# Performance work log

Measured on AMD Instinct MI355X. Metric: run time of the kernel, lower is better.

## Reference

```python
import jax, jax.numpy as jnp
import numpy as np

D_MODEL, D_K, D_V, H = 512, 64, 64, 8
B, NQ, NK = 2, 2048, 2048


def setup_inputs() -> dict:
    key = jax.random.key(0)
    ks = jax.random.split(key, 12)
    inp = {
        "queries": jax.random.normal(ks[0], (B, NQ, D_MODEL), jnp.float32),
        "keys": jax.random.normal(ks[1], (B, NK, D_MODEL), jnp.float32),
        "values": jax.random.normal(ks[2], (B, NK, D_MODEL), jnp.float32),
        "attention_weights": jax.random.uniform(ks[3], (B, H, NQ, NK), jnp.float32),
        # causal mask: True above the diagonal => masked (every row keeps >=1 entry)
        "attention_mask": jnp.broadcast_to(
            jnp.triu(jnp.ones((NQ, NK), dtype=bool), k=1), (B, H, NQ, NK)
        ),
        # linear params, torch Linear convention: W [out, in], b [out]
        "Wq": 0.001 * jax.random.normal(ks[4], (H * D_K, D_MODEL), jnp.float32),
        "bq": jnp.zeros((H * D_K,), jnp.float32),
        "Wk": 0.001 * jax.random.normal(ks[5], (H * D_K, D_MODEL), jnp.float32),
        "bk": jnp.zeros((H * D_K,), jnp.float32),
        "Wv": 0.001 * jax.random.normal(ks[6], (H * D_V, D_MODEL), jnp.float32),
        "bv": jnp.zeros((H * D_V,), jnp.float32),
        "Wo": 0.001 * jax.random.normal(ks[7], (D_MODEL, H * D_V), jnp.float32),
        "bo": jnp.zeros((D_MODEL,), jnp.float32),
    }
    return inp


def reference(queries, keys, values, attention_weights, attention_mask,
              Wq, bq, Wk, bk, Wv, bv, Wo, bo):
    b_s, nq, _ = queries.shape
    nk = keys.shape[1]
    # projections -> (b, h, n, d)
    q = (queries @ Wq.T + bq).reshape(b_s, nq, H, D_K).transpose(0, 2, 1, 3)
    k = (keys @ Wk.T + bk).reshape(b_s, nk, H, D_K).transpose(0, 2, 1, 3)
    v = (values @ Wv.T + bv).reshape(b_s, nk, H, D_V).transpose(0, 2, 1, 3)
    att = jnp.einsum('bhqd,bhkd->bhqk', q, k) / np.sqrt(D_K).astype(np.float32)
    att = att * attention_weights
    att = jnp.where(attention_mask, -jnp.inf, att)
    att = jax.nn.softmax(att, axis=-1)  # dropout p=0 => identity (eval)
    out = jnp.einsum('bhqk,bhkd->bhqd', att, v)
    out = out.transpose(0, 2, 1, 3).reshape(b_s, nq, H * D_V)
    return out @ Wo.T + bo
```

## Files before the change

kernel.cpp:

```cpp
#include <hip/hip_runtime.h>


typedef unsigned short u16;
typedef unsigned int u32;
typedef __bf16 bf16x8 __attribute__((ext_vector_type(8)));
typedef float f32x4 __attribute__((ext_vector_type(4)));

#define NQTILES 32

__device__ inline u16 f2bf(float f) {
    u32 x = __builtin_bit_cast(u32, f);
    u32 r = (x + 0x7fffu + ((x >> 16) & 1u)) >> 16;
    return (u16)r;
}

__device__ inline f32x4 mfma16(bf16x8 a, bf16x8 b, f32x4 c) {
    return __builtin_amdgcn_mfma_f32_16x16x32_bf16(a, b, c, 0, 0, 0);
}

__device__ inline void gload16(const void* g, void* l) {
    __builtin_amdgcn_global_load_lds((const __attribute__((address_space(1))) void*)g,
                                     (__attribute__((address_space(3))) void*)l, 16, 0, 0);
}

__device__ inline void stage_swz(const u16* __restrict__ src, int ld, int nrows,
                                 char* lds, int tid) {
    int lane = tid & 63;
    int total = nrows * 8;
    for (int p = tid; p < total; p += 256) {
        int row = p >> 3;
        int seg = (p & 7) ^ (row & 7);
        const char* g = (const char*)(src + (size_t)row * ld) + (seg << 4);
        char* l = lds + ((size_t)(p - lane) << 4);
        gload16(g, l);
    }
}

__device__ inline bf16x8 ldsf(const char* lds, int row, int seg) {
    return *(const bf16x8*)(lds + row * 128 + (((seg ^ (row & 7)) & 7) << 4));
}

__device__ inline void loadw(float (&w)[16], const float* __restrict__ wgt, size_t wbase,
                             int q0, int k0, int wrow, int lg, int lc) {
#pragma unroll
    for (int c = 0; c < 4; ++c)
#pragma unroll
        for (int r = 0; r < 4; ++r)
            w[c * 4 + r] =
                wgt[wbase + (size_t)(q0 + wrow + lg * 4 + r) * 2048 + k0 + c * 16 + lc];
}

__global__ __launch_bounds__(256) void convert_kernel(
    const float* __restrict__ q, const float* __restrict__ k, const float* __restrict__ v,
    const float* __restrict__ wq, const float* __restrict__ wk, const float* __restrict__ wv,
    const float* __restrict__ wo, u16* __restrict__ dst) {
    size_t i = ((size_t)blockIdx.x * 256 + threadIdx.x) * 8;
    if (i >= 7340032) return;
    const float* src; size_t off;
    if      (i < 2097152) { src = q;  off = i; }
    else if (i < 4194304) { src = k;  off = i - 2097152; }
    else if (i < 6291456) { src = v;  off = i - 4194304; }
    else if (i < 6553600) { src = wq; off = i - 6291456; }
    else if (i < 6815744) { src = wk; off = i - 6553600; }
    else if (i < 7077888) { src = wv; off = i - 6815744; }
    else                  { src = wo; off = i - 7077888; }
    float4 a = *(const float4*)(src + off);
    float4 b = *(const float4*)(src + off + 4);
    uint4 pk;
    pk.x = f2bf(a.x) | ((u32)f2bf(a.y) << 16);
    pk.y = f2bf(a.z) | ((u32)f2bf(a.w) << 16);
    pk.z = f2bf(b.x) | ((u32)f2bf(b.y) << 16);
    pk.w = f2bf(b.z) | ((u32)f2bf(b.w) << 16);
    *(uint4*)(dst + i) = pk;
}

__device__ inline void gemm_core(const u16* __restrict__ A, const u16* __restrict__ W,
                                 const float* __restrict__ bias,
                                 u16* __restrict__ outB, float* __restrict__ outF,
                                 char (*Alds)[16384], char (*Blds)[16384],
                                 int bx, int by, int tid) {
    const int lane = tid & 63, wid = tid >> 6;
    const int wr = wid >> 1, wc = wid & 1;
    const int lg = lane >> 4, lc = lane & 15;
    const int brow = by * 128, bcol = bx * 128;
    f32x4 acc[4][4] = {};
    stage_swz(A + (size_t)brow * 512, 512, 128, Alds[0], tid);
    stage_swz(W + (size_t)bcol * 512, 512, 128, Blds[0], tid);
    __syncthreads();
    for (int kt = 0; kt < 8; ++kt) {
        const int cur = kt & 1;
        if (kt < 7) {
            stage_swz(A + (size_t)brow * 512 + (kt + 1) * 64, 512, 128, Alds[cur ^ 1], tid);
            stage_swz(W + (size_t)bcol * 512 + (kt + 1) * 64, 512, 128, Blds[cur ^ 1], tid);
        }
#pragma unroll
        for (int s = 0; s < 2; ++s) {
            bf16x8 af[4], bf[4];
#pragma unroll
            for (int m = 0; m < 4; ++m) af[m] = ldsf(Alds[cur], wr * 64 + m * 16 + lc, s * 4 + lg);
#pragma unroll
            for (int n = 0; n < 4; ++n) bf[n] = ldsf(Blds[cur], wc * 64 + n * 16 + lc, s * 4 + lg);
#pragma unroll
            for (int m = 0; m < 4; ++m)
#pragma unroll
                for (int n = 0; n < 4; ++n)
                    acc[m][n] = mfma16(af[m], bf[n], acc[m][n]);
        }
        __syncthreads();
    }
#pragma unroll
    for (int n = 0; n < 4; ++n) {
        int gcol = bcol + wc * 64 + n * 16 + lc;
        float bv = bias[gcol];
#pragma unroll
        for (int m = 0; m < 4; ++m) {
            int grow0 = brow + wr * 64 + m * 16 + lg * 4;
#pragma unroll
            for (int r = 0; r < 4; ++r) {
                float v = acc[m][n][r] + bv;
                if (outF) outF[(size_t)(grow0 + r) * 512 + gcol] = v;
                else      outB[(size_t)(grow0 + r) * 512 + gcol] = f2bf(v);
            }
        }
    }
}

__global__ __launch_bounds__(256, 2) void gemm_qkv_kernel(
    const u16* __restrict__ qx, const u16* __restrict__ kx, const u16* __restrict__ vx,
    const u16* __restrict__ wq, const u16* __restrict__ wk, const u16* __restrict__ wv,
    const float* __restrict__ bq, const float* __restrict__ bk, const float* __restrict__ bv,
    u16* __restrict__ qp, u16* __restrict__ kp, u16* __restrict__ vp) {
    __shared__ __attribute__((aligned(16))) char Alds[2][16384];
    __shared__ __attribute__((aligned(16))) char Blds[2][16384];
    int z = blockIdx.z;
    const u16* A = (z == 0) ? qx : (z == 1) ? kx : vx;
    const u16* W = (z == 0) ? wq : (z == 1) ? wk : wv;
    const float* bias = (z == 0) ? bq : (z == 1) ? bk : bv;
    u16* out = (z == 0) ? qp : (z == 1) ? kp : vp;
    gemm_core(A, W, bias, out, nullptr, Alds, Blds, blockIdx.x, blockIdx.y, threadIdx.x);
}

__global__ __launch_bounds__(256, 2) void gemm_out_kernel(
    const u16* __restrict__ ob, const u16* __restrict__ wo,
    const float* __restrict__ bo, float* __restrict__ out) {
    __shared__ __attribute__((aligned(16))) char Alds[2][16384];
    __shared__ __attribute__((aligned(16))) char Blds[2][16384];
    gemm_core(ob, wo, bo, nullptr, out, Alds, Blds, blockIdx.x, blockIdx.y, threadIdx.x);
}

__global__ __launch_bounds__(256) void vtrans_kernel(const u16* __restrict__ vp,
                                                     u16* __restrict__ vt) {
    __shared__ __attribute__((aligned(16))) u16 t[64 * 64];
    int tid = threadIdx.x, lane = tid & 63;
    int nt = blockIdx.x;
    int bh = blockIdx.y;
    int b = bh >> 3, h = bh & 7;
    for (int ii = 0; ii < 2; ++ii) {
        int p = ii * 256 + tid;
        int nrow = p >> 3, seg = p & 7;
        const char* g = (const char*)(vp + ((size_t)(b * 2048 + nt * 64 + nrow)) * 512 + h * 64)
                        + (seg << 4);
        char* l = (char*)t + ((size_t)(p - lane) << 4);
        gload16(g, l);
    }
    __syncthreads();
    for (int ii = 0; ii < 2; ++ii) {
        int idx = ii * 256 + tid;
        int d = idx >> 3;
        int nseg = idx & 7;
        u16 tmp[8];
#pragma unroll
        for (int j = 0; j < 8; ++j) tmp[j] = t[(nseg * 8 + j) * 64 + d];
        uint4 pk;
        pk.x = tmp[0] | ((u32)tmp[1] << 16);
        pk.y = tmp[2] | ((u32)tmp[3] << 16);
        pk.z = tmp[4] | ((u32)tmp[5] << 16);
        pk.w = tmp[6] | ((u32)tmp[7] << 16);
        *(uint4*)(vt + ((size_t)(bh * 64 + d)) * 2048 + nt * 64 + nseg * 8) = pk;
    }
}

__global__ __launch_bounds__(256, 2) void attn_kernel(
    const u16* __restrict__ qp, const u16* __restrict__ kp, const u16* __restrict__ vt,
    const float* __restrict__ wgt, u16* __restrict__ ob) {
    __shared__ __attribute__((aligned(16))) char kbuf[2][8192];
    __shared__ __attribute__((aligned(16))) char vbuf[2][8192];
    __shared__ __attribute__((aligned(16))) char pbuf[8192];
    const int tid = threadIdx.x, lane = tid & 63, wid = tid >> 6;
    const int lg = lane >> 4, lc = lane & 15;
    const int bid = blockIdx.x;
    const int rank = bid >> 4;
    const int bh = bid & 15;
    const int it = (NQTILES - 1) - rank;
    const int b = bh >> 3, h = bh & 7;
    const int q0 = it * 64;
    const int wrow = wid * 16;
    const size_t wbase = ((size_t)(b * 8 + h)) * 2048 * 2048;
    const size_t vtb0 = ((size_t)(bh * 64)) * 2048;

    stage_swz(qp + ((size_t)(b * 2048 + q0)) * 512 + h * 64, 512, 64, pbuf, tid);
    stage_swz(kp + ((size_t)(b * 2048)) * 512 + h * 64, 512, 64, kbuf[0], tid);
    stage_swz(vt + vtb0, 2048, 64, vbuf[0], tid);
    float wcur[16], wnxt[16];
    loadw(wcur, wgt, wbase, q0, 0, wrow, lg, lc);
#pragma unroll
    for (int i = 0; i < 16; ++i) wnxt[i] = 0.f;
    __syncthreads();
    bf16x8 qf[2];
#pragma unroll
    for (int s = 0; s < 2; ++s) qf[s] = ldsf(pbuf, wrow + lc, s * 4 + lg);

    float mrow[4], lrow[4];
#pragma unroll
    for (int r = 0; r < 4; ++r) { mrow[r] = -1e30f; lrow[r] = 0.f; }
    f32x4 oacc[4] = {};

    for (int j = 0; j <= it; ++j) {
        const int cur = j & 1;
        if (j < it) {
            stage_swz(kp + ((size_t)(b * 2048 + (j + 1) * 64)) * 512 + h * 64, 512, 64,
                      kbuf[cur ^ 1], tid);
            stage_swz(vt + vtb0 + (j + 1) * 64, 2048, 64, vbuf[cur ^ 1], tid);
            loadw(wnxt, wgt, wbase, q0, (j + 1) * 64, wrow, lg, lc);
        }

        f32x4 sacc[4] = {};
#pragma unroll
        for (int s = 0; s < 2; ++s) {
            bf16x8 kf[4];
#pragma unroll
            for (int c = 0; c < 4; ++c) kf[c] = ldsf(kbuf[cur], c * 16 + lc, s * 4 + lg);
#pragma unroll
            for (int c = 0; c < 4; ++c) sacc[c] = mfma16(qf[s], kf[c], sacc[c]);
        }

#pragma unroll
        for (int r = 0; r < 4; ++r) {
            float mx = -1e30f;
#pragma unroll
            for (int c = 0; c < 4; ++c) {
                float sv = sacc[c][r] * 0.125f * wcur[c * 4 + r];
                if (j == it) {
                    int qq = wrow + lg * 4 + r, kk = c * 16 + lc;
                    if (kk > qq) sv = -1e30f;
                }
                sacc[c][r] = sv;
                mx = fmaxf(mx, sv);
            }
            mx = fmaxf(mx, __shfl_xor(mx, 1));
            mx = fmaxf(mx, __shfl_xor(mx, 2));
            mx = fmaxf(mx, __shfl_xor(mx, 4));
            mx = fmaxf(mx, __shfl_xor(mx, 8));
            float mnew = fmaxf(mrow[r], mx);
            float sc = __expf(mrow[r] - mnew);
            float sum = 0.f;
#pragma unroll
            for (int c = 0; c < 4; ++c) {
                float e = __expf(sacc[c][r] - mnew);
                sacc[c][r] = e;
                sum += e;
            }
            sum += __shfl_xor(sum, 1);
            sum += __shfl_xor(sum, 2);
            sum += __shfl_xor(sum, 4);
            sum += __shfl_xor(sum, 8);
            lrow[r] = lrow[r] * sc + sum;
            mrow[r] = mnew;
#pragma unroll
            for (int c = 0; c < 4; ++c) oacc[c][r] *= sc;
        }

#pragma unroll
        for (int c = 0; c < 4; ++c)
#pragma unroll
            for (int r = 0; r < 4; ++r) {
                int row = wrow + lg * 4 + r;
                int byte = (c * 16 + lc) * 2;
                *(u16*)(pbuf + row * 128 + (byte ^ ((row & 7) << 4))) = f2bf(sacc[c][r]);
            }

        bf16x8 pa[2];
#pragma unroll
        for (int s = 0; s < 2; ++s) pa[s] = ldsf(pbuf, wrow + lc, s * 4 + lg);
#pragma unroll
        for (int c = 0; c < 4; ++c)
#pragma unroll
            for (int s = 0; s < 2; ++s) {
                bf16x8 vf = ldsf(vbuf[cur], c * 16 + lc, s * 4 + lg);
                oacc[c] = mfma16(pa[s], vf, oacc[c]);
            }
        __syncthreads();
        if (j < it) {
#pragma unroll
            for (int i = 0; i < 16; ++i) wcur[i] = wnxt[i];
        }
    }

#pragma unroll
    for (int r = 0; r < 4; ++r) {
        float inv = 1.f / lrow[r];
        int qq = q0 + wrow + lg * 4 + r;
        size_t base = ((size_t)(b * 2048 + qq)) * 512 + h * 64;
#pragma unroll
        for (int c = 0; c < 4; ++c)
            ob[base + c * 16 + lc] = f2bf(oacc[c][r] * inv);
    }
}

extern "C" void kernel_launch(void* const* d_in, const int* in_sizes, int n_in,
                              void* d_out, int out_size, void* d_ws, size_t ws_size,
                              hipStream_t stream) {
    const float* q   = (const float*)d_in[0];
    const float* k   = (const float*)d_in[1];
    const float* v   = (const float*)d_in[2];
    const float* wgt = (const float*)d_in[3];
    const float* Wq = (const float*)d_in[5];
    const float* bq = (const float*)d_in[6];
    const float* Wk = (const float*)d_in[7];
    const float* bk = (const float*)d_in[8];
    const float* Wv = (const float*)d_in[9];
    const float* bv = (const float*)d_in[10];
    const float* Wo = (const float*)d_in[11];
    const float* bo = (const float*)d_in[12];
    float* out = (float*)d_out;

    u16* ws  = (u16*)d_ws;
    u16* qx  = ws;
    u16* kx  = qx  + 2097152;
    u16* vx  = kx  + 2097152;
    u16* wqb = vx  + 2097152;
    u16* wkb = wqb + 262144;
    u16* wvb = wkb + 262144;
    u16* wob = wvb + 262144;
    u16* qp  = wob + 262144;
    u16* kp  = qp  + 2097152;
    u16* vp  = kp  + 2097152;
    u16* vtb = vp  + 2097152;
    u16* ob  = vtb + 2097152;

    convert_kernel<<<3584, 256, 0, stream>>>(q, k, v, Wq, Wk, Wv, Wo, qx);
    gemm_qkv_kernel<<<dim3(4, 32, 3), 256, 0, stream>>>(qx, kx, vx, wqb, wkb, wvb,
                                                        bq, bk, bv, qp, kp, vp);
    vtrans_kernel<<<dim3(32, 16), 256, 0, stream>>>(vp, vtb);
    attn_kernel<<<512, 256, 0, stream>>>(qp, kp, vtb, wgt, ob);
    gemm_out_kernel<<<dim3(4, 32, 1), 256, 0, stream>>>(ob, wob, bo, out);
}
```

Baseline: 541.0 us.

## Fuse fp32-to-bf16 conversion and V transpose into projection GEMMs

Removes the separate convert kernel and the V transpose kernel. The QKV and output GEMMs now load fp32 inputs and weights into registers, convert them to bf16, and write the result to swizzled LDS while the MFMAs of the previous tile run. The V projection writes its output directly in transposed layout. This drops two launches and the round trips of the bf16 intermediates through global memory. In exchange it doubles global read bytes inside the GEMMs, raises register pressure, and the transposed V stores are only 8-byte scattered writes.

```diff
diff --git a/kernel.cpp b/kernel.cpp
--- a/kernel.cpp
+++ b/kernel.cpp
@@ -40,6 +40,32 @@
     return *(const bf16x8*)(lds + row * 128 + (((seg ^ (row & 7)) & 7) << 4));
 }
 
+__device__ inline void ldf32(const float* __restrict__ src, int tid, float4 (&h)[8]) {
+#pragma unroll
+    for (int k = 0; k < 4; ++k) {
+        int p = tid + 256 * k;
+        int row = p >> 3, seg = p & 7;
+        const float4* g = (const float4*)(src + (size_t)row * 512 + seg * 8);
+        h[2 * k]     = g[0];
+        h[2 * k + 1] = g[1];
+    }
+}
+
+__device__ inline void wrstage(const float4 (&h)[8], char* lds, int tid) {
+#pragma unroll
+    for (int k = 0; k < 4; ++k) {
+        int p = tid + 256 * k;
+        int row = p >> 3, seg = (p & 7) ^ (row & 7);
+        float4 a = h[2 * k], b = h[2 * k + 1];
+        uint4 pk;
+        pk.x = f2bf(a.x) | ((u32)f2bf(a.y) << 16);
+        pk.y = f2bf(a.z) | ((u32)f2bf(a.w) << 16);
+        pk.z = f2bf(b.x) | ((u32)f2bf(b.y) << 16);
+        pk.w = f2bf(b.z) | ((u32)f2bf(b.w) << 16);
+        *(uint4*)(lds + row * 128 + (seg << 4)) = pk;
+    }
+}
+
 __device__ inline void loadw(float (&w)[16], const float* __restrict__ wgt, size_t wbase,
                              int q0, int k0, int wrow, int lg, int lc) {
 #pragma unroll
@@ -50,48 +76,34 @@
                 wgt[wbase + (size_t)(q0 + wrow + lg * 4 + r) * 2048 + k0 + c * 16 + lc];
 }
 
-__global__ __launch_bounds__(256) void convert_kernel(
+__global__ __launch_bounds__(256, 2) void gemm_qkvt_kernel(
     const float* __restrict__ q, const float* __restrict__ k, const float* __restrict__ v,
     const float* __restrict__ wq, const float* __restrict__ wk, const float* __restrict__ wv,
-    const float* __restrict__ wo, u16* __restrict__ dst) {
-    size_t i = ((size_t)blockIdx.x * 256 + threadIdx.x) * 8;
-    if (i >= 7340032) return;
-    const float* src; size_t off;
-    if      (i < 2097152) { src = q;  off = i; }
-    else if (i < 4194304) { src = k;  off = i - 2097152; }
-    else if (i < 6291456) { src = v;  off = i - 4194304; }
-    else if (i < 6553600) { src = wq; off = i - 6291456; }
-    else if (i < 6815744) { src = wk; off = i - 6553600; }
-    else if (i < 7077888) { src = wv; off = i - 6815744; }
-    else                  { src = wo; off = i - 7077888; }
-    float4 a = *(const float4*)(src + off);
-    float4 b = *(const float4*)(src + off + 4);
-    uint4 pk;
-    pk.x = f2bf(a.x) | ((u32)f2bf(a.y) << 16);
-    pk.y = f2bf(a.z) | ((u32)f2bf(a.w) << 16);
-    pk.z = f2bf(b.x) | ((u32)f2bf(b.y) << 16);
-    pk.w = f2bf(b.z) | ((u32)f2bf(b.w) << 16);
-    *(uint4*)(dst + i) = pk;
-}
-
-__device__ inline void gemm_core(const u16* __restrict__ A, const u16* __restrict__ W,
-                                 const float* __restrict__ bias,
-                                 u16* __restrict__ outB, float* __restrict__ outF,
-                                 char (*Alds)[16384], char (*Blds)[16384],
-                                 int bx, int by, int tid) {
-    const int lane = tid & 63, wid = tid >> 6;
+    const float* __restrict__ bq, const float* __restrict__ bk, const float* __restrict__ bv,
+    u16* __restrict__ qp, u16* __restrict__ kp, u16* __restrict__ vt) {
+    __shared__ __attribute__((aligned(16))) char Alds[2][16384];
+    __shared__ __attribute__((aligned(16))) char Blds[2][16384];
+    const int z = blockIdx.z;
+    const float* A = (z == 0) ? q : (z == 1) ? k : v;
+    const float* W = (z == 0) ? wq : (z == 1) ? wk : wv;
+    const float* bias = (z == 0) ? bq : (z == 1) ? bk : bv;
+    const int tid = threadIdx.x, lane = tid & 63, wid = tid >> 6;
     const int wr = wid >> 1, wc = wid & 1;
     const int lg = lane >> 4, lc = lane & 15;
-    const int brow = by * 128, bcol = bx * 128;
+    const int brow = blockIdx.y * 128, bcol = blockIdx.x * 128;
     f32x4 acc[4][4] = {};
-    stage_swz(A + (size_t)brow * 512, 512, 128, Alds[0], tid);
-    stage_swz(W + (size_t)bcol * 512, 512, 128, Blds[0], tid);
+    float4 ha[8], hw[8];
+
+    ldf32(A + (size_t)brow * 512, tid, ha);
+    ldf32(W + (size_t)bcol * 512, tid, hw);
+    wrstage(ha, Alds[0], tid);
+    wrstage(hw, Blds[0], tid);
     __syncthreads();
     for (int kt = 0; kt < 8; ++kt) {
         const int cur = kt & 1;
         if (kt < 7) {
-            stage_swz(A + (size_t)brow * 512 + (kt + 1) * 64, 512, 128, Alds[cur ^ 1], tid);
-            stage_swz(W + (size_t)bcol * 512 + (kt + 1) * 64, 512, 128, Blds[cur ^ 1], tid);
+            ldf32(A + (size_t)brow * 512 + (kt + 1) * 64, tid, ha);
+            ldf32(W + (size_t)bcol * 512 + (kt + 1) * 64, tid, hw);
         }
 #pragma unroll
         for (int s = 0; s < 2; ++s) {
@@ -106,77 +118,98 @@
                 for (int n = 0; n < 4; ++n)
                     acc[m][n] = mfma16(af[m], bf[n], acc[m][n]);
         }
+        if (kt < 7) {
+            wrstage(ha, Alds[cur ^ 1], tid);
+            wrstage(hw, Blds[cur ^ 1], tid);
+        }
         __syncthreads();
     }
-#pragma unroll
-    for (int n = 0; n < 4; ++n) {
-        int gcol = bcol + wc * 64 + n * 16 + lc;
-        float bv = bias[gcol];
-#pragma unroll
-        for (int m = 0; m < 4; ++m) {
-            int grow0 = brow + wr * 64 + m * 16 + lg * 4;
-#pragma unroll
-            for (int r = 0; r < 4; ++r) {
-                float v = acc[m][n][r] + bv;
-                if (outF) outF[(size_t)(grow0 + r) * 512 + gcol] = v;
-                else      outB[(size_t)(grow0 + r) * 512 + gcol] = f2bf(v);
-            }
-        }
-    }
-}
-
-__global__ __launch_bounds__(256, 2) void gemm_qkv_kernel(
-    const u16* __restrict__ qx, const u16* __restrict__ kx, const u16* __restrict__ vx,
-    const u16* __restrict__ wq, const u16* __restrict__ wk, const u16* __restrict__ wv,
-    const float* __restrict__ bq, const float* __restrict__ bk, const float* __restrict__ bv,
-    u16* __restrict__ qp, u16* __restrict__ kp, u16* __restrict__ vp) {
-    __shared__ __attribute__((aligned(16))) char Alds[2][16384];
-    __shared__ __attribute__((aligned(16))) char Blds[2][16384];
-    int z = blockIdx.z;
-    const u16* A = (z == 0) ? qx : (z == 1) ? kx : vx;
-    const u16* W = (z == 0) ? wq : (z == 1) ? wk : wv;
-    const float* bias = (z == 0) ? bq : (z == 1) ? bk : bv;
-    u16* out = (z == 0) ? qp : (z == 1) ? kp : vp;
-    gemm_core(A, W, bias, out, nullptr, Alds, Blds, blockIdx.x, blockIdx.y, threadIdx.x);
+
+    if (z < 2) {
+        u16* out = (z == 0) ? qp : kp;
+#pragma unroll
+        for (int n = 0; n < 4; ++n) {
+            int gcol = bcol + wc * 64 + n * 16 + lc;
+            float bvv = bias[gcol];
+#pragma unroll
+            for (int m = 0; m < 4; ++m) {
+                int grow0 = brow + wr * 64 + m * 16 + lg * 4;
+#pragma unroll
+                for (int r = 0; r < 4; ++r)
+                    out[(size_t)(grow0 + r) * 512 + gcol] = f2bf(acc[m][n][r] + bvv);
+            }
+        }
+    } else {
+        const int b = brow >> 11;
+        const int nbase = (brow & 2047) + wr * 64;
+#pragma unroll
+        for (int n = 0; n < 4; ++n) {
+            int gcol = bcol + wc * 64 + n * 16 + lc;
+            float bvv = bias[gcol];
+            size_t rowbase = ((size_t)(b * 512 + gcol)) * 2048;
+#pragma unroll
+            for (int m = 0; m < 4; ++m) {
+                int n0 = nbase + m * 16 + lg * 4;
+                ushort4 s;
+                s.x = f2bf(acc[m][n][0] + bvv);
+                s.y = f2bf(acc[m][n][1] + bvv);
+                s.z = f2bf(acc[m][n][2] + bvv);
+                s.w = f2bf(acc[m][n][3] + bvv);
+                *(ushort4*)(vt + rowbase + n0) = s;
+            }
+        }
+    }
 }
 
 __global__ __launch_bounds__(256, 2) void gemm_out_kernel(
-    const u16* __restrict__ ob, const u16* __restrict__ wo,
+    const u16* __restrict__ ob, const float* __restrict__ wo,
     const float* __restrict__ bo, float* __restrict__ out) {
     __shared__ __attribute__((aligned(16))) char Alds[2][16384];
     __shared__ __attribute__((aligned(16))) char Blds[2][16384];
-    gemm_core(ob, wo, bo, nullptr, out, Alds, Blds, blockIdx.x, blockIdx.y, threadIdx.x);
-}
-
-__global__ __launch_bounds__(256) void vtrans_kernel(const u16* __restrict__ vp,
-                                                     u16* __restrict__ vt) {
-    __shared__ __attribute__((aligned(16))) u16 t[64 * 64];
-    int tid = threadIdx.x, lane = tid & 63;
-    int nt = blockIdx.x;
-    int bh = blockIdx.y;
-    int b = bh >> 3, h = bh & 7;
-    for (int ii = 0; ii < 2; ++ii) {
-        int p = ii * 256 + tid;
-        int nrow = p >> 3, seg = p & 7;
-        const char* g = (const char*)(vp + ((size_t)(b * 2048 + nt * 64 + nrow)) * 512 + h * 64)
-                        + (seg << 4);
-        char* l = (char*)t + ((size_t)(p - lane) << 4);
-        gload16(g, l);
-    }
+    const int tid = threadIdx.x, lane = tid & 63, wid = tid >> 6;
+    const int wr = wid >> 1, wc = wid & 1;
+    const int lg = lane >> 4, lc = lane & 15;
+    const int brow = blockIdx.y * 128, bcol = blockIdx.x * 128;
+    f32x4 acc[4][4] = {};
+    float4 hw[8];
+
+    stage_swz(ob + (size_t)brow * 512, 512, 128, Alds[0], tid);
+    ldf32(wo + (size_t)bcol * 512, tid, hw);
+    wrstage(hw, Blds[0], tid);
     __syncthreads();
-    for (int ii = 0; ii < 2; ++ii) {
-        int idx = ii * 256 + tid;
-        int d = idx >> 3;
-        int nseg = idx & 7;
-        u16 tmp[8];
-#pragma unroll
-        for (int j = 0; j < 8; ++j) tmp[j] = t[(nseg * 8 + j) * 64 + d];
-        uint4 pk;
-        pk.x = tmp[0] | ((u32)tmp[1] << 16);
-        pk.y = tmp[2] | ((u32)tmp[3] << 16);
-        pk.z = tmp[4] | ((u32)tmp[5] << 16);
-        pk.w = tmp[6] | ((u32)tmp[7] << 16);
-        *(uint4*)(vt + ((size_t)(bh * 64 + d)) * 2048 + nt * 64 + nseg * 8) = pk;
+    for (int kt = 0; kt < 8; ++kt) {
+        const int cur = kt & 1;
+        if (kt < 7) {
+            stage_swz(ob + (size_t)brow * 512 + (kt + 1) * 64, 512, 128, Alds[cur ^ 1], tid);
+            ldf32(wo + (size_t)bcol * 512 + (kt + 1) * 64, tid, hw);
+        }
+#pragma unroll
+        for (int s = 0; s < 2; ++s) {
+            bf16x8 af[4], bf[4];
+#pragma unroll
+            for (int m = 0; m < 4; ++m) af[m] = ldsf(Alds[cur], wr * 64 + m * 16 + lc, s * 4 + lg);
+#pragma unroll
+            for (int n = 0; n < 4; ++n) bf[n] = ldsf(Blds[cur], wc * 64 + n * 16 + lc, s * 4 + lg);
+#pragma unroll
+            for (int m = 0; m < 4; ++m)
+#pragma unroll
+                for (int n = 0; n < 4; ++n)
+                    acc[m][n] = mfma16(af[m], bf[n], acc[m][n]);
+        }
+        if (kt < 7) wrstage(hw, Blds[cur ^ 1], tid);
+        __syncthreads();
+    }
+#pragma unroll
+    for (int n = 0; n < 4; ++n) {
+        int gcol = bcol + wc * 64 + n * 16 + lc;
+        float bvv = bo[gcol];
+#pragma unroll
+        for (int m = 0; m < 4; ++m) {
+            int grow0 = brow + wr * 64 + m * 16 + lg * 4;
+#pragma unroll
+            for (int r = 0; r < 4; ++r)
+                out[(size_t)(grow0 + r) * 512 + gcol] = acc[m][n][r] + bvv;
+        }
     }
 }
 
@@ -325,23 +358,13 @@
     float* out = (float*)d_out;
 
     u16* ws  = (u16*)d_ws;
-    u16* qx  = ws;
-    u16* kx  = qx  + 2097152;
-    u16* vx  = kx  + 2097152;
-    u16* wqb = vx  + 2097152;
-    u16* wkb = wqb + 262144;
-    u16* wvb = wkb + 262144;
-    u16* wob = wvb + 262144;
-    u16* qp  = wob + 262144;
+    u16* qp  = ws;
     u16* kp  = qp  + 2097152;
-    u16* vp  = kp  + 2097152;
-    u16* vtb = vp  + 2097152;
+    u16* vtb = kp  + 2097152;
     u16* ob  = vtb + 2097152;
 
-    convert_kernel<<<3584, 256, 0, stream>>>(q, k, v, Wq, Wk, Wv, Wo, qx);
-    gemm_qkv_kernel<<<dim3(4, 32, 3), 256, 0, stream>>>(qx, kx, vx, wqb, wkb, wvb,
-                                                        bq, bk, bv, qp, kp, vp);
-    vtrans_kernel<<<dim3(32, 16), 256, 0, stream>>>(vp, vtb);
+    gemm_qkvt_kernel<<<dim3(4, 32, 3), 256, 0, stream>>>(q, k, v, Wq, Wk, Wv,
+                                                         bq, bk, bv, qp, kp, vtb);
     attn_kernel<<<512, 256, 0, stream>>>(qp, kp, vtb, wgt, ob);
-    gemm_out_kernel<<<dim3(4, 32, 1), 256, 0, stream>>>(ob, wob, bo, out);
-}
+    gemm_out_kernel<<<dim3(4, 32), 256, 0, stream>>>(ob, Wo, bo, out);
+}
```

Measured after the change: 547.0 us. No clear change (+1.1%).
